# Kernel optimization log

Hardware: AMD Instinct MI355X
Metric: run time of the kernel (lower is better)

Reference implementation:

```python
import jax, jax.numpy as jnp
import numpy as np

B, TQ, TK, E, H, DH = 4, 1024, 1024, 1024, 16, 64
EPS = 1e-5

def setup_inputs() -> dict:
    key = jax.random.key(0)
    ks = jax.random.split(key, 16)
    s = 0.02
    return {
        "x": jax.random.normal(ks[0], (B, TQ, E), jnp.float32),
        "encoder_out": jax.random.normal(ks[1], (B, TK, E), jnp.float32),
        "Q1w": jax.random.normal(ks[2], (H, DH, E), jnp.float32) * s,
        "Q1b": jax.random.normal(ks[3], (H, DH), jnp.float32) * s,
        "Q2w": jax.random.normal(ks[4], (H, DH, E), jnp.float32) * s,
        "Q2b": jax.random.normal(ks[5], (H, DH), jnp.float32) * s,
        "K1w": jax.random.normal(ks[6], (H, DH, E), jnp.float32) * s,
        "K1b": jax.random.normal(ks[7], (H, DH), jnp.float32) * s,
        "K2w": jax.random.normal(ks[8], (H, DH, E), jnp.float32) * s,
        "K2b": jax.random.normal(ks[9], (H, DH), jnp.float32) * s,
        "Vw": jax.random.normal(ks[10], (H, DH, E), jnp.float32) * s,
        "Vb": jax.random.normal(ks[11], (H, DH), jnp.float32) * s,
        "lam": jax.random.uniform(ks[12], (H,), jnp.float32, 0.5, 1.0),
        "gn_gamma": jnp.ones((H * DH,), jnp.float32),
        "gn_beta": jnp.zeros((H * DH,), jnp.float32),
        "out_w": jax.random.normal(ks[13], (E, H * DH), jnp.float32) * s,
        "out_b": jax.random.normal(ks[14], (E,), jnp.float32) * s,
    }

def _proj(inp, w, b):
    # inp: [B,T,E], w: [H,DH,E] -> [B,H,T,DH]
    return jnp.einsum('bte,hde->bhtd', inp, w) + b[None, :, None, :]

def reference(x, encoder_out, Q1w, Q1b, Q2w, Q2b, K1w, K1b, K2w, K2b, Vw, Vb,
              lam, gn_gamma, gn_beta, out_w, out_b):
    scale = 1.0 / jnp.sqrt(jnp.float32(DH))
    q1 = _proj(x, Q1w, Q1b)
    q2 = _proj(x, Q2w, Q2b)
    k1 = _proj(encoder_out, K1w, K1b)
    k2 = _proj(encoder_out, K2w, K2b)
    v = _proj(encoder_out, Vw, Vb)
    s1 = jnp.einsum('bhtd,bhsd->bhts', q1, k1) * scale  # [B,H,TQ,TK]
    s2 = jnp.einsum('bhtd,bhsd->bhts', q2, k2) * scale
    w = jax.nn.softmax(s1, axis=-1) - lam[None, :, None, None] * jax.nn.softmax(s2, axis=-1)
    out = jnp.einsum('bhts,bhsd->bhtd', w, v)  # [B,H,TQ,DH]
    # GroupNorm(num_groups=H, channels=H*DH) over [B,C,T]: per (B,H) stats over (T,DH)
    mu = jnp.mean(out, axis=(2, 3), keepdims=True)
    var = jnp.mean(jnp.square(out - mu), axis=(2, 3), keepdims=True)
    normed = (out - mu) * jax.lax.rsqrt(var + EPS)
    g = gn_gamma.reshape(H, DH)[None, :, None, :]
    b_ = gn_beta.reshape(H, DH)[None, :, None, :]
    normed = normed * g + b_
    y = normed.transpose(0, 2, 1, 3).reshape(B, TQ, H * DH)
    return y @ out_w.T + out_b
```

## Files before the change

kernel.cpp:

```cpp
#include <hip/hip_runtime.h>
#include <cmath>

typedef __bf16 bf16_t;
typedef bf16_t bf16x8 __attribute__((ext_vector_type(8)));
typedef bf16_t bf16x4 __attribute__((ext_vector_type(4)));
typedef float  f32x4  __attribute__((ext_vector_type(4)));
typedef float  f32x16 __attribute__((ext_vector_type(16)));
typedef unsigned int u32x4v __attribute__((ext_vector_type(4)));

#define Bn  4
#define TQn 1024
#define TKn 1024
#define En  1024
#define Hn  16
#define DHn 64

static constexpr float EPSv = 1e-5f;
static constexpr float C_SCALE = 0.18033688011112042f;

#define GLDS16(g, l)                                                         \
    __builtin_amdgcn_global_load_lds(                                        \
        (const __attribute__((address_space(1))) void*)(g),                  \
        (__attribute__((address_space(3))) void*)(l), 16, 0, 0)

__global__ __launch_bounds__(256)
void cvt_all(const float* __restrict__ x, const float* __restrict__ enc,
             const float* __restrict__ q1w, const float* __restrict__ q2w,
             const float* __restrict__ k1w, const float* __restrict__ k2w,
             const float* __restrict__ vw,  const float* __restrict__ outw,
             bf16_t* __restrict__ xb, bf16_t* __restrict__ encb,
             bf16_t* __restrict__ wq, bf16_t* __restrict__ wkv,
             bf16_t* __restrict__ wob)
{
    int idx = blockIdx.x * 256 + threadIdx.x;
    const float* src; bf16_t* dst;
    if      (idx < 1048576) { src = x    + (size_t)idx * 4;              dst = xb   + (size_t)idx * 4; }
    else if (idx < 2097152) { src = enc  + (size_t)(idx - 1048576) * 4;  dst = encb + (size_t)(idx - 1048576) * 4; }
    else if (idx < 2359296) { src = q1w  + (size_t)(idx - 2097152) * 4;  dst = wq   + (size_t)(idx - 2097152) * 4; }
    else if (idx < 2621440) { src = q2w  + (size_t)(idx - 2359296) * 4;  dst = wq   + 1048576 + (size_t)(idx - 2359296) * 4; }
    else if (idx < 2883584) { src = k1w  + (size_t)(idx - 2621440) * 4;  dst = wkv  + (size_t)(idx - 2621440) * 4; }
    else if (idx < 3145728) { src = k2w  + (size_t)(idx - 2883584) * 4;  dst = wkv  + 1048576 + (size_t)(idx - 2883584) * 4; }
    else if (idx < 3407872) { src = vw   + (size_t)(idx - 3145728) * 4;  dst = wkv  + 2097152 + (size_t)(idx - 3145728) * 4; }
    else                    { src = outw + (size_t)(idx - 3407872) * 4;  dst = wob  + (size_t)(idx - 3407872) * 4; }
    float4 v = *(const float4*)src;
    bf16x4 o;
    o[0] = (bf16_t)v.x; o[1] = (bf16_t)v.y; o[2] = (bf16_t)v.z; o[3] = (bf16_t)v.w;
    *(bf16x4*)dst = o;
}

__global__ __launch_bounds__(256, 4)
void gemm_proj(const bf16_t* __restrict__ xb, const bf16_t* __restrict__ encb,
               const bf16_t* __restrict__ wq, const bf16_t* __restrict__ wkv,
               const float* __restrict__ q1b, const float* __restrict__ q2b,
               const float* __restrict__ k1b, const float* __restrict__ k2b,
               const float* __restrict__ vb,
               bf16_t* __restrict__ q12, bf16_t* __restrict__ k12v)
{
    __shared__ __align__(16) bf16_t sAB[2][128 * 64];
    bf16_t* const sA = &sAB[0][0];
    bf16_t* const sB = &sAB[1][0];
    bf16_t* const sC = &sAB[0][0];

    int bx = blockIdx.x;
    const int blockM = blockIdx.y << 7;
    const bf16_t* A; const bf16_t* W; bf16_t* C; const float* bp; int blockN;
    if (bx < 16) {
        A = xb; W = wq; C = q12; blockN = bx << 7;
        bp = (blockN >> 10) ? q2b : q1b;
    } else {
        bx -= 16;
        A = encb; W = wkv; C = k12v; blockN = bx << 7;
        const int seg0 = blockN >> 10;
        bp = (seg0 == 0) ? k1b : ((seg0 == 1) ? k2b : vb);
    }

    const int tid = threadIdx.x;
    const int w = tid >> 6, lane = tid & 63;
    const int q = lane >> 4, r = lane & 15;
    const int wm = w & 1, wn = w >> 1;

    f32x4 acc[4][4];
#pragma unroll
    for (int i = 0; i < 4; ++i)
#pragma unroll
        for (int j = 0; j < 4; ++j) acc[i][j] = (f32x4){0.f, 0.f, 0.f, 0.f};

    for (int k0 = 0; k0 < 1024; k0 += 64) {
#pragma unroll
        for (int c = 0; c < 4; ++c) {
            const int s = c * 256 + tid;
            const int row = s >> 3;
            const int cg = (s & 7) ^ (row & 7);
            GLDS16(A + (size_t)(blockM + row) * 1024 + k0 + cg * 8, sA + c * 2048 + w * 512);
            GLDS16(W + (size_t)(blockN + row) * 1024 + k0 + cg * 8, sB + c * 2048 + w * 512);
        }
        __syncthreads();
#pragma unroll
        for (int ks = 0; ks < 2; ++ks) {
            bf16x8 a[4], b[4];
#pragma unroll
            for (int i = 0; i < 4; ++i) {
                const int row = wm * 64 + i * 16 + r;
                const int g = (ks * 4 + q) ^ (row & 7);
                a[i] = *(const bf16x8*)&sA[row * 64 + g * 8];
            }
#pragma unroll
            for (int j = 0; j < 4; ++j) {
                const int row = wn * 64 + j * 16 + r;
                const int g = (ks * 4 + q) ^ (row & 7);
                b[j] = *(const bf16x8*)&sB[row * 64 + g * 8];
            }
#pragma unroll
            for (int i = 0; i < 4; ++i)
#pragma unroll
                for (int j = 0; j < 4; ++j)
                    acc[i][j] = __builtin_amdgcn_mfma_f32_16x16x32_bf16(a[i], b[j], acc[i][j], 0, 0, 0);
        }
        __syncthreads();
    }

#pragma unroll
    for (int j = 0; j < 4; ++j) {
        const int n = wn * 64 + j * 16 + r;
        const float bv = bp[(blockN + n) & 1023];
#pragma unroll
        for (int i = 0; i < 4; ++i) {
            f32x4 v = acc[i][j];
#pragma unroll
            for (int e = 0; e < 4; ++e) {
                const int m = wm * 64 + i * 16 + q * 4 + e;
                sC[m * 128 + (((n >> 3) ^ (m & 7)) << 3) + (n & 7)] = (bf16_t)(v[e] + bv);
            }
        }
    }
    __syncthreads();
    const int seg = blockN >> 10;
#pragma unroll
    for (int v8 = 0; v8 < 8; ++v8) {
        const int flat = v8 * 256 + tid;
        const int m = flat >> 4;
        const int nb = flat & 15;
        bf16x8 row = *(const bf16x8*)&sC[m * 128 + ((nb ^ (m & 7)) << 3)];
        const int gm = blockM + m, gn = blockN + nb * 8;
        const int bb = gm >> 10, t = gm & 1023;
        const int h = (gn >> 6) & 15, d = gn & 63;
        *(bf16x8*)&C[((((size_t)seg * 4 + bb) * 16 + h) * 1024 + t) * 64 + d] = row;
    }
}

__global__ __launch_bounds__(256, 4)
void gemm_out_gn(const bf16_t* __restrict__ attnb, const float* __restrict__ stats,
                 const float* __restrict__ gamma, const float* __restrict__ beta,
                 const bf16_t* __restrict__ wob, const float* __restrict__ outb,
                 float* __restrict__ out)
{
    __shared__ __align__(16) bf16_t sA[64 * 64];
    __shared__ __align__(16) bf16_t sB[128 * 64];
    __shared__ float sCa[1024];
    __shared__ float sCb[1024];
    __shared__ float sMu[16], sRs[16];

    const int L = blockIdx.x;
    const int xcd = L & 7, kk = L >> 3;
    const int blockM = (xcd * 8 + (kk >> 3)) * 64;
    const int blockN = (kk & 7) * 128;
    const int b = blockM >> 10;

    const int tid = threadIdx.x;
    const int w = tid >> 6, lane = tid & 63;
    const int q = lane >> 4, r = lane & 15;

    if (tid < 16) {
        const int bh = b * 16 + tid;
        float s1 = 0.f, s2 = 0.f;
#pragma unroll
        for (int k = 0; k < 8; ++k) { s1 += stats[bh * 8 + k]; s2 += stats[512 + bh * 8 + k]; }
        const float mu = s1 * (1.f / 65536.f);
        const float var = s2 * (1.f / 65536.f) - mu * mu;
        sMu[tid] = mu;
        sRs[tid] = rsqrtf(var + EPSv);
    }
    __syncthreads();
#pragma unroll
    for (int u = 0; u < 4; ++u) {
        const int c = u * 256 + tid;
        const int h = c >> 6;
        const float a = sRs[h] * gamma[c];
        sCa[c] = a;
        sCb[c] = beta[c] - sMu[h] * a;
    }
    __syncthreads();

    f32x4 acc[4][2];
#pragma unroll
    for (int i = 0; i < 4; ++i)
#pragma unroll
        for (int j = 0; j < 2; ++j) acc[i][j] = (f32x4){0.f, 0.f, 0.f, 0.f};

    for (int k0 = 0; k0 < 1024; k0 += 64) {
        const int h = k0 >> 6;
#pragma unroll
        for (int c = 0; c < 2; ++c) {
            const int s = c * 256 + tid;
            const int row = s >> 3;
            const int cb = s & 7;
            const int t = (blockM + row) & 1023;
            bf16x8 v = *(const bf16x8*)(attnb + ((size_t)(b * 16 + h) << 16) + t * 64 + cb * 8);
            const int cbase = h * 64 + cb * 8;
            f32x4 ca0 = *(const f32x4*)&sCa[cbase];
            f32x4 ca1 = *(const f32x4*)&sCa[cbase + 4];
            f32x4 cb0 = *(const f32x4*)&sCb[cbase];
            f32x4 cb1 = *(const f32x4*)&sCb[cbase + 4];
            bf16x8 o;
#pragma unroll
            for (int i = 0; i < 4; ++i) {
                o[i]     = (bf16_t)((float)v[i]     * ca0[i] + cb0[i]);
                o[i + 4] = (bf16_t)((float)v[i + 4] * ca1[i] + cb1[i]);
            }
            *(bf16x8*)&sA[row * 64 + ((cb ^ (row & 7)) << 3)] = o;
        }
#pragma unroll
        for (int c = 0; c < 4; ++c) {
            const int s = c * 256 + tid;
            const int row = s >> 3;
            const int cg = (s & 7) ^ (row & 7);
            GLDS16(wob + (size_t)(blockN + row) * 1024 + k0 + cg * 8, sB + c * 2048 + w * 512);
        }
        __syncthreads();
#pragma unroll
        for (int ks = 0; ks < 2; ++ks) {
            bf16x8 a[4], bfr[2];
#pragma unroll
            for (int i = 0; i < 4; ++i) {
                const int row = i * 16 + r;
                const int g = (ks * 4 + q) ^ (row & 7);
                a[i] = *(const bf16x8*)&sA[row * 64 + g * 8];
            }
#pragma unroll
            for (int j = 0; j < 2; ++j) {
                const int row = w * 32 + j * 16 + r;
                const int g = (ks * 4 + q) ^ (row & 7);
                bfr[j] = *(const bf16x8*)&sB[row * 64 + g * 8];
            }
#pragma unroll
            for (int i = 0; i < 4; ++i)
#pragma unroll
                for (int j = 0; j < 2; ++j)
                    acc[i][j] = __builtin_amdgcn_mfma_f32_16x16x32_bf16(a[i], bfr[j], acc[i][j], 0, 0, 0);
        }
        __syncthreads();
    }

#pragma unroll
    for (int j = 0; j < 2; ++j) {
        const int n = blockN + w * 32 + j * 16 + r;
        const float bv = outb[n];
#pragma unroll
        for (int i = 0; i < 4; ++i) {
            f32x4 v = acc[i][j];
#pragma unroll
            for (int e = 0; e < 4; ++e) {
                const int m = blockM + i * 16 + q * 4 + e;
                out[(size_t)m * 1024 + n] = v[e] + bv;
            }
        }
    }
}

__device__ __forceinline__ unsigned cvtpk_bf16(float a, float b)
{
    unsigned r;
    asm("v_cvt_pk_bf16_f32 %0, %1, %2" : "=v"(r) : "v"(a), "v"(b));
    return r;
}

__device__ __forceinline__ void pack_pa(const f32x16& p, bf16x8& pa0, bf16x8& pa1)
{
    unsigned a0 = cvtpk_bf16(p[0], p[1]),   b0 = cvtpk_bf16(p[4], p[5]);
    asm("v_permlane32_swap_b32 %0, %1" : "+v"(a0), "+v"(b0));
    unsigned a1 = cvtpk_bf16(p[2], p[3]),   b1 = cvtpk_bf16(p[6], p[7]);
    asm("v_permlane32_swap_b32 %0, %1" : "+v"(a1), "+v"(b1));
    pa0 = __builtin_bit_cast(bf16x8, (u32x4v){a0, a1, b0, b1});
    unsigned a2 = cvtpk_bf16(p[8], p[9]),   b2 = cvtpk_bf16(p[12], p[13]);
    asm("v_permlane32_swap_b32 %0, %1" : "+v"(a2), "+v"(b2));
    unsigned a3 = cvtpk_bf16(p[10], p[11]), b3 = cvtpk_bf16(p[14], p[15]);
    asm("v_permlane32_swap_b32 %0, %1" : "+v"(a3), "+v"(b3));
    pa1 = __builtin_bit_cast(bf16x8, (u32x4v){a2, a3, b2, b3});
}

__global__ __launch_bounds__(512, 4)
void diff_attn32(const bf16_t* __restrict__ q12, const bf16_t* __restrict__ k12v,
                 const float* __restrict__ lam, bf16_t* __restrict__ out,
                 float* __restrict__ stats)
{
    __shared__ __align__(16) bf16_t arena[24576];
    bf16_t* const sK1 = arena;
    bf16_t* const sK2 = arena + 8192;
    bf16_t* const sVt = arena + 16384;
    float*  const xchg = (float*)arena;
    __shared__ float sl[2][128];
    __shared__ float sred[16];

    const int tid = threadIdx.x;
    const int w = tid >> 6, lane = tid & 63;
    const int st_id = w >> 2, wv = w & 3;
    const int hi = lane >> 5, lo = lane & 31;
    const int bh = blockIdx.x, qt = blockIdx.y;
    const float lamv = lam[bh & (Hn - 1)];

    const size_t HT = (size_t)TKn * DHn;
    const bf16_t* qg  = q12 + (size_t)(st_id * 64 + bh) * HT + (size_t)qt * 128 * DHn;
    const bf16_t* k1g = k12v + (size_t)bh * HT;
    const bf16_t* k2g = k1g + 64 * HT;
    const bf16_t* vg  = k1g + 128 * HT;
    const bf16_t* const sKs = st_id ? sK2 : sK1;

    bf16x8 fQ[4];
#pragma unroll
    for (int dk = 0; dk < 4; ++dk)
        fQ[dk] = *(const bf16x8*)(qg + (size_t)(wv * 32 + lo) * 64 + dk * 16 + hi * 8);

    f32x16 O0, O1;
#pragma unroll
    for (int e = 0; e < 16; ++e) { O0[e] = 0.f; O1[e] = 0.f; }
    float lsum = 0.f;

    {
        const int row = tid >> 3;
        const int cg = (tid & 7) ^ (row & 7);
        GLDS16(k1g + row * 64 + cg * 8, sK1 + tid * 8);
        GLDS16(k2g + row * 64 + cg * 8, sK2 + tid * 8);
        const int s = tid & 63;
        bf16x8 v0 = *(const bf16x8*)(vg + (size_t)s * 64 + w * 8);
#pragma unroll
        for (int i = 0; i < 8; ++i) {
            const int d = w * 8 + i;
            sVt[d * 64 + (((s >> 3) ^ i) << 3) + (s & 7)] = v0[i];
        }
        __syncthreads();
    }

    for (int st = 0; st < TKn / 64; ++st) {
        const int cur = st & 1, nxt = cur ^ 1;
        bf16x8 vr;
        if (st < 15) {
            const int row = tid >> 3;
            const int cg = (tid & 7) ^ (row & 7);
            GLDS16(k1g + (size_t)(st + 1) * 4096 + row * 64 + cg * 8, sK1 + nxt * 4096 + tid * 8);
            GLDS16(k2g + (size_t)(st + 1) * 4096 + row * 64 + cg * 8, sK2 + nxt * 4096 + tid * 8);
            vr = *(const bf16x8*)(vg + (size_t)(st + 1) * 4096 + (size_t)(tid & 63) * 64 + w * 8);
        }

        const bf16_t* sKc = sKs + cur * 4096;
        const bf16_t* sVc = sVt + cur * 4096;
#pragma unroll
        for (int kb = 0; kb < 2; ++kb) {
            f32x16 S;
#pragma unroll
            for (int e = 0; e < 16; ++e) S[e] = 0.f;
            __builtin_amdgcn_s_setprio(1);
#pragma unroll
            for (int dk = 0; dk < 4; ++dk) {
                bf16x8 fk = *(const bf16x8*)&sKc[(kb * 32 + lo) * 64 + (((dk * 2 + hi) ^ (lo & 7)) << 3)];
                S = __builtin_amdgcn_mfma_f32_32x32x16_bf16(fk, fQ[dk], S, 0, 0, 0);
            }
            __builtin_amdgcn_s_setprio(0);
#pragma unroll
            for (int e = 0; e < 16; ++e) {
                S[e] = __builtin_amdgcn_exp2f(S[e] * C_SCALE);
                lsum += S[e];
            }
            bf16x8 pa0, pa1;
            pack_pa(S, pa0, pa1);
            const int c0 = ((kb * 4 + hi) ^ (lo & 7)) << 3;
            const int c1 = ((kb * 4 + 2 + hi) ^ (lo & 7)) << 3;
            bf16x8 fv00 = *(const bf16x8*)&sVc[(0 * 32 + lo) * 64 + c0];
            bf16x8 fv01 = *(const bf16x8*)&sVc[(0 * 32 + lo) * 64 + c1];
            bf16x8 fv10 = *(const bf16x8*)&sVc[(1 * 32 + lo) * 64 + c0];
            bf16x8 fv11 = *(const bf16x8*)&sVc[(1 * 32 + lo) * 64 + c1];
            __builtin_amdgcn_s_setprio(1);
            O0 = __builtin_amdgcn_mfma_f32_32x32x16_bf16(pa0, fv00, O0, 0, 0, 0);
            O0 = __builtin_amdgcn_mfma_f32_32x32x16_bf16(pa1, fv01, O0, 0, 0, 0);
            O1 = __builtin_amdgcn_mfma_f32_32x32x16_bf16(pa0, fv10, O1, 0, 0, 0);
            O1 = __builtin_amdgcn_mfma_f32_32x32x16_bf16(pa1, fv11, O1, 0, 0, 0);
            __builtin_amdgcn_s_setprio(0);
        }

        if (st < 15) {
            const int s = tid & 63;
#pragma unroll
            for (int i = 0; i < 8; ++i) {
                const int d = w * 8 + i;
                sVt[nxt * 4096 + d * 64 + (((s >> 3) ^ i) << 3) + (s & 7)] = vr[i];
            }
        }
        __syncthreads();
    }

    lsum += __shfl_xor(lsum, 32);
    if (hi == 0) sl[st_id][wv * 32 + lo] = lsum;

    if (st_id == 1) {
#pragma unroll
        for (int reg = 0; reg < 16; ++reg) {
            const int t = wv * 32 + (reg & 3) + 8 * (reg >> 2) + 4 * hi;
            const float inv2 = lamv / sl[1][t];
            xchg[t * 64 + lo]      = O0[reg] * inv2;
            xchg[t * 64 + 32 + lo] = O1[reg] * inv2;
        }
    }
    __syncthreads();

    if (st_id == 0) {
        float ssum = 0.f, ssq = 0.f;
        bf16_t* op = out + ((size_t)bh * TQn + (size_t)qt * 128) * DHn;
#pragma unroll
        for (int reg = 0; reg < 16; ++reg) {
            const int t = wv * 32 + (reg & 3) + 8 * (reg >> 2) + 4 * hi;
            const float inv1 = 1.0f / sl[0][t];
            const float o0 = O0[reg] * inv1 - xchg[t * 64 + lo];
            const float o1 = O1[reg] * inv1 - xchg[t * 64 + 32 + lo];
            op[(size_t)t * 64 + lo]      = (bf16_t)o0;
            op[(size_t)t * 64 + 32 + lo] = (bf16_t)o1;
            ssum += o0 + o1;
            ssq  += o0 * o0 + o1 * o1;
        }
#pragma unroll
        for (int d = 1; d < 64; d <<= 1) {
            ssum += __shfl_xor(ssum, d);
            ssq  += __shfl_xor(ssq, d);
        }
        if (lane == 0) { sred[wv] = ssum; sred[8 + wv] = ssq; }
    }
    __syncthreads();
    if (tid == 0) {
        stats[(bh << 3) + qt]       = sred[0] + sred[1] + sred[2] + sred[3];
        stats[512 + (bh << 3) + qt] = sred[8] + sred[9] + sred[10] + sred[11];
    }
}

extern "C" void kernel_launch(void* const* d_in, const int* in_sizes, int n_in,
                              void* d_out, int out_size, void* d_ws, size_t ws_size,
                              hipStream_t stream)
{
    const float* x    = (const float*)d_in[0];
    const float* enc  = (const float*)d_in[1];
    const float* Q1w  = (const float*)d_in[2];
    const float* Q1b  = (const float*)d_in[3];
    const float* Q2w  = (const float*)d_in[4];
    const float* Q2b  = (const float*)d_in[5];
    const float* K1w  = (const float*)d_in[6];
    const float* K1b  = (const float*)d_in[7];
    const float* K2w  = (const float*)d_in[8];
    const float* K2b  = (const float*)d_in[9];
    const float* Vw   = (const float*)d_in[10];
    const float* Vb   = (const float*)d_in[11];
    const float* lam  = (const float*)d_in[12];
    const float* gng  = (const float*)d_in[13];
    const float* gnb  = (const float*)d_in[14];
    const float* outw = (const float*)d_in[15];
    const float* outb = (const float*)d_in[16];
    float* out = (float*)d_out;

    bf16_t* xb   = (bf16_t*)d_ws;
    bf16_t* encb = xb   + 4194304;
    bf16_t* wq   = encb + 4194304;
    bf16_t* wkv  = wq   + 2097152;
    bf16_t* wob  = wkv  + 3145728;
    bf16_t* q12  = wob  + 1048576;
    bf16_t* k12v = q12  + 8388608;
    bf16_t* attnb= xb;
    float*  stats= (float*)wq;

    cvt_all<<<14336, 256, 0, stream>>>(x, enc, Q1w, Q2w, K1w, K2w, Vw, outw,
                                       xb, encb, wq, wkv, wob);

    gemm_proj<<<dim3(40, 32), 256, 0, stream>>>(xb, encb, wq, wkv,
                                                Q1b, Q2b, K1b, K2b, Vb, q12, k12v);

    diff_attn32<<<dim3(64, 8), 512, 0, stream>>>(q12, k12v, lam, attnb, stats);

    gemm_out_gn<<<512, 256, 0, stream>>>(attnb, stats, gng, gnb, wob, outb, out);
}
```

Measured before the change: 246.4 us.

## Double attention KV tile to 128 keys and remap projection GEMM blocks per XCD

```diff
diff --git a/kernel.cpp b/kernel.cpp
--- a/kernel.cpp
+++ b/kernel.cpp
@@ -61,8 +61,11 @@
     bf16_t* const sB = &sAB[1][0];
     bf16_t* const sC = &sAB[0][0];
 
-    int bx = blockIdx.x;
-    const int blockM = blockIdx.y << 7;
+    const int L = blockIdx.x;
+    const int xcd = L & 7, o = L >> 3;
+    int bx = (xcd & 3) * 10 + (o % 10);
+    const int blockM = ((xcd >> 2) * 16 + (o / 10)) << 7;
+
     const bf16_t* A; const bf16_t* W; bf16_t* C; const float* bp; int blockN;
     if (bx < 16) {
         A = xb; W = wq; C = q12; blockN = bx << 7;
@@ -288,15 +291,15 @@
     pa1 = __builtin_bit_cast(bf16x8, (u32x4v){a2, a3, b2, b3});
 }
 
-__global__ __launch_bounds__(512, 4)
+__global__ __launch_bounds__(512, 2)
 void diff_attn32(const bf16_t* __restrict__ q12, const bf16_t* __restrict__ k12v,
                  const float* __restrict__ lam, bf16_t* __restrict__ out,
                  float* __restrict__ stats)
 {
-    __shared__ __align__(16) bf16_t arena[24576];
+    __shared__ __align__(16) bf16_t arena[49152];
     bf16_t* const sK1 = arena;
-    bf16_t* const sK2 = arena + 8192;
-    bf16_t* const sVt = arena + 16384;
+    bf16_t* const sK2 = arena + 16384;
+    bf16_t* const sVt = arena + 32768;
     float*  const xchg = (float*)arena;
     __shared__ float sl[2][128];
     __shared__ float sred[16];
@@ -315,6 +318,9 @@
     const bf16_t* vg  = k1g + 128 * HT;
     const bf16_t* const sKs = st_id ? sK2 : sK1;
 
+    const int vs = tid & 127;
+    const int vdg = tid >> 7;
+
     bf16x8 fQ[4];
 #pragma unroll
     for (int dk = 0; dk < 4; ++dk)
@@ -326,35 +332,50 @@
     float lsum = 0.f;
 
     {
-        const int row = tid >> 3;
-        const int cg = (tid & 7) ^ (row & 7);
-        GLDS16(k1g + row * 64 + cg * 8, sK1 + tid * 8);
-        GLDS16(k2g + row * 64 + cg * 8, sK2 + tid * 8);
-        const int s = tid & 63;
-        bf16x8 v0 = *(const bf16x8*)(vg + (size_t)s * 64 + w * 8);
-#pragma unroll
-        for (int i = 0; i < 8; ++i) {
-            const int d = w * 8 + i;
-            sVt[d * 64 + (((s >> 3) ^ i) << 3) + (s & 7)] = v0[i];
-        }
+#pragma unroll
+        for (int c = 0; c < 2; ++c) {
+            const int s = c * 512 + tid;
+            const int row = s >> 3;
+            const int cg = (s & 7) ^ (row & 7);
+            GLDS16(k1g + row * 64 + cg * 8, sK1 + s * 8);
+            GLDS16(k2g + row * 64 + cg * 8, sK2 + s * 8);
+        }
+        bf16x8 v0[2];
+#pragma unroll
+        for (int rep = 0; rep < 2; ++rep)
+            v0[rep] = *(const bf16x8*)(vg + (size_t)vs * 64 + vdg * 16 + rep * 8);
+#pragma unroll
+        for (int rep = 0; rep < 2; ++rep)
+#pragma unroll
+            for (int i = 0; i < 8; ++i) {
+                const int d = vdg * 16 + rep * 8 + i;
+                sVt[d * 128 + (((vs >> 3) ^ i) << 3) + (vs & 7)] = v0[rep][i];
+            }
         __syncthreads();
     }
 
-    for (int st = 0; st < TKn / 64; ++st) {
+    for (int st = 0; st < TKn / 128; ++st) {
         const int cur = st & 1, nxt = cur ^ 1;
-        bf16x8 vr;
-        if (st < 15) {
-            const int row = tid >> 3;
-            const int cg = (tid & 7) ^ (row & 7);
-            GLDS16(k1g + (size_t)(st + 1) * 4096 + row * 64 + cg * 8, sK1 + nxt * 4096 + tid * 8);
-            GLDS16(k2g + (size_t)(st + 1) * 4096 + row * 64 + cg * 8, sK2 + nxt * 4096 + tid * 8);
-            vr = *(const bf16x8*)(vg + (size_t)(st + 1) * 4096 + (size_t)(tid & 63) * 64 + w * 8);
-        }
-
-        const bf16_t* sKc = sKs + cur * 4096;
-        const bf16_t* sVc = sVt + cur * 4096;
-#pragma unroll
-        for (int kb = 0; kb < 2; ++kb) {
+        bf16x8 vr[2];
+        if (st < 7) {
+#pragma unroll
+            for (int c = 0; c < 2; ++c) {
+                const int s = c * 512 + tid;
+                const int row = s >> 3;
+                const int cg = (s & 7) ^ (row & 7);
+                GLDS16(k1g + (size_t)(st + 1) * 8192 + row * 64 + cg * 8, sK1 + nxt * 8192 + s * 8);
+                GLDS16(k2g + (size_t)(st + 1) * 8192 + row * 64 + cg * 8, sK2 + nxt * 8192 + s * 8);
+            }
+            const bf16_t* vp = vg + (size_t)(st + 1) * 8192;
+#pragma unroll
+            for (int rep = 0; rep < 2; ++rep)
+                vr[rep] = *(const bf16x8*)(vp + (size_t)vs * 64 + vdg * 16 + rep * 8);
+        }
+
+        const bf16_t* sKc = sKs + cur * 8192;
+        const bf16_t* sVc = sVt + cur * 8192;
+#pragma unroll
+        for (int kb = 0; kb < 4; ++kb) {
             f32x16 S;
 #pragma unroll
             for (int e = 0; e < 16; ++e) S[e] = 0.f;
@@ -372,12 +393,12 @@
             }
             bf16x8 pa0, pa1;
             pack_pa(S, pa0, pa1);
-            const int c0 = ((kb * 4 + hi) ^ (lo & 7)) << 3;
-            const int c1 = ((kb * 4 + 2 + hi) ^ (lo & 7)) << 3;
-            bf16x8 fv00 = *(const bf16x8*)&sVc[(0 * 32 + lo) * 64 + c0];
-            bf16x8 fv01 = *(const bf16x8*)&sVc[(0 * 32 + lo) * 64 + c1];
-            bf16x8 fv10 = *(const bf16x8*)&sVc[(1 * 32 + lo) * 64 + c0];
-            bf16x8 fv11 = *(const bf16x8*)&sVc[(1 * 32 + lo) * 64 + c1];
+            const int g0 = ((kb * 4 + hi) ^ (lo & 7)) << 3;
+            const int g1 = ((kb * 4 + 2 + hi) ^ (lo & 7)) << 3;
+            bf16x8 fv00 = *(const bf16x8*)&sVc[(0 * 32 + lo) * 128 + g0];
+            bf16x8 fv01 = *(const bf16x8*)&sVc[(0 * 32 + lo) * 128 + g1];
+            bf16x8 fv10 = *(const bf16x8*)&sVc[(1 * 32 + lo) * 128 + g0];
+            bf16x8 fv11 = *(const bf16x8*)&sVc[(1 * 32 + lo) * 128 + g1];
             __builtin_amdgcn_s_setprio(1);
             O0 = __builtin_amdgcn_mfma_f32_32x32x16_bf16(pa0, fv00, O0, 0, 0, 0);
             O0 = __builtin_amdgcn_mfma_f32_32x32x16_bf16(pa1, fv01, O0, 0, 0, 0);
@@ -386,13 +407,14 @@
             __builtin_amdgcn_s_setprio(0);
         }
 
-        if (st < 15) {
-            const int s = tid & 63;
-#pragma unroll
-            for (int i = 0; i < 8; ++i) {
-                const int d = w * 8 + i;
-                sVt[nxt * 4096 + d * 64 + (((s >> 3) ^ i) << 3) + (s & 7)] = vr[i];
-            }
+        if (st < 7) {
+#pragma unroll
+            for (int rep = 0; rep < 2; ++rep)
+#pragma unroll
+                for (int i = 0; i < 8; ++i) {
+                    const int d = vdg * 16 + rep * 8 + i;
+                    sVt[nxt * 8192 + d * 128 + (((vs >> 3) ^ i) << 3) + (vs & 7)] = vr[rep][i];
+                }
         }
         __syncthreads();
     }
@@ -475,8 +497,8 @@
     cvt_all<<<14336, 256, 0, stream>>>(x, enc, Q1w, Q2w, K1w, K2w, Vw, outw,
                                        xb, encb, wq, wkv, wob);
 
-    gemm_proj<<<dim3(40, 32), 256, 0, stream>>>(xb, encb, wq, wkv,
-                                                Q1b, Q2b, K1b, K2b, Vb, q12, k12v);
+    gemm_proj<<<1280, 256, 0, stream>>>(xb, encb, wq, wkv,
+                                        Q1b, Q2b, K1b, K2b, Vb, q12, k12v);
 
     diff_attn32<<<dim3(64, 8), 512, 0, stream>>>(q12, k12v, lam, attnb, stats);
 
```

After: 243.5 us. Within noise of the previous version (-1.2%).
